# Performance work log

Measured on AMD Instinct MI355X. Metric: run time of the kernel, lower is better.

The kernel has to match this reference:

```python
import jax, jax.numpy as jnp
import numpy as np

B, SWIN_D, VIT_D, E, H = 16384, 768, 512, 1024, 4
HD = E // H  # 256


def setup_inputs() -> dict:
    key = jax.random.key(0)
    ks = jax.random.split(key, 12)
    s = lambda fan_in: 1.0 / np.sqrt(fan_in)
    return {
        "swin_feat": jax.random.normal(ks[0], (B, SWIN_D), jnp.float32),
        "vit_feat": jax.random.normal(ks[1], (B, VIT_D), jnp.float32),
        # outer projections (nn.Linear: y = x @ W.T + b)
        "Wq": jax.random.uniform(ks[2], (E, SWIN_D), jnp.float32, -s(SWIN_D), s(SWIN_D)),
        "bq": jax.random.uniform(ks[3], (E,), jnp.float32, -s(SWIN_D), s(SWIN_D)),
        "Wk": jax.random.uniform(ks[4], (E, VIT_D), jnp.float32, -s(VIT_D), s(VIT_D)),
        "bk": jax.random.uniform(ks[5], (E,), jnp.float32, -s(VIT_D), s(VIT_D)),
        "Wv": jax.random.uniform(ks[6], (E, VIT_D), jnp.float32, -s(VIT_D), s(VIT_D)),
        "bv": jax.random.uniform(ks[7], (E,), jnp.float32, -s(VIT_D), s(VIT_D)),
        # nn.MultiheadAttention internal in_proj (stacked q,k,v) and out_proj
        "in_proj_w": jax.random.uniform(ks[8], (3 * E, E), jnp.float32, -s(E), s(E)),
        "in_proj_b": jnp.zeros((3 * E,), jnp.float32),
        "Wo": jax.random.uniform(ks[9], (E, E), jnp.float32, -s(E), s(E)),
        "bo": jnp.zeros((E,), jnp.float32),
    }


def reference(swin_feat, vit_feat, Wq, bq, Wk, bk, Wv, bv, in_proj_w, in_proj_b, Wo, bo):
    # outer projections -> [B, E] (seq_len = 1, so the seq dim is implicit)
    q = swin_feat @ Wq.T + bq
    k = vit_feat @ Wk.T + bk
    v = vit_feat @ Wv.T + bv
    # MultiheadAttention in-projection (split stacked weight)
    Wiq, Wik, Wiv = in_proj_w[:E], in_proj_w[E:2 * E], in_proj_w[2 * E:]
    biq, bik, biv = in_proj_b[:E], in_proj_b[E:2 * E], in_proj_b[2 * E:]
    q2 = (q @ Wiq.T + biq).reshape(B, H, HD)
    k2 = (k @ Wik.T + bik).reshape(B, H, HD)
    v2 = (v @ Wiv.T + biv).reshape(B, H, HD)
    # attention with q_len = kv_len = 1
    scale = 1.0 / np.sqrt(HD)
    scores = jnp.einsum('bhd,bhd->bh', q2, k2) * scale        # [B, H]
    w = jax.nn.softmax(scores[..., None], axis=-1)             # softmax over 1 key -> ones
    attn = w * v2                                              # [B, H, HD]
    out = attn.reshape(B, E) @ Wo.T + bo                       # out-projection
    return out
```

## Files before the change

kernel.cpp:

```cpp
#include <hip/hip_runtime.h>
#include <stdint.h>
#include <stddef.h>

#define E_DIM 1024

typedef __bf16 v8bf __attribute__((ext_vector_type(8)));
typedef float v4f __attribute__((ext_vector_type(4)));

__device__ __forceinline__ unsigned short f2bf(float x) {
  unsigned int u = __builtin_bit_cast(unsigned int, x);
  u += 0x7fffu + ((u >> 16) & 1u);
  return (unsigned short)(u >> 16);
}

template <int RB>
__device__ __forceinline__ int swz(int r, int c) {
  if constexpr (RB >= 128) return c ^ ((r & 7) << 4);
  else return c;
}

template <int N>
__device__ __forceinline__ void waitcnt_vm() {
  static_assert(N == 0 || N == 4 || N == 8 || N == 12, "add literal");
  if constexpr (N == 0)  asm volatile("s_waitcnt vmcnt(0)" ::: "memory");
  if constexpr (N == 4)  asm volatile("s_waitcnt vmcnt(4)" ::: "memory");
  if constexpr (N == 8)  asm volatile("s_waitcnt vmcnt(8)" ::: "memory");
  if constexpr (N == 12) asm volatile("s_waitcnt vmcnt(12)" ::: "memory");
}

template <int ROWS, int BK>
__device__ __forceinline__ void stageg(const unsigned short* __restrict__ G, int g0,
                                       int ldg, int k0, char* L, int wid, int lane) {
  constexpr int RB = BK * 2;
  constexpr int ITERS = (ROWS * RB) / 4096;
#pragma unroll
  for (int it = 0; it < ITERS; ++it) {
    int lbase = it * 4096 + wid * 1024;
    int lin = lbase + lane * 16;
    int r = lin / RB, cb = lin % RB;
    int gcb = swz<RB>(r, cb);
    const char* g = (const char*)G + ((size_t)(g0 + r) * ldg + k0) * 2 + gcb;
    __builtin_amdgcn_global_load_lds((const __attribute__((address_space(1))) void*)g,
                                     (__attribute__((address_space(3))) void*)(L + lbase),
                                     16, 0, 0);
  }
}

template <int RB>
__device__ __forceinline__ v8bf frag_bf16(const char* L, int r, int kelem) {
  int o = swz<RB>(r, kelem * 2);
  return *(const v8bf*)(L + r * RB + o);
}

template <int BM, int BN, int BK, int FM, int FN>
__device__ __forceinline__ void compute_tile(const char* Al, const char* Bl,
                                             v4f (&acc)[FM][FN],
                                             int wr, int wc, int lr, int kg) {
  constexpr int RBA = BK * 2, RBB = BK * 2;
  constexpr int TMW = BM / 2, TNW = BN / 2;
#pragma unroll
  for (int kk = 0; kk < BK / 32; ++kk) {
    const int ke = kk * 32 + kg * 8;
    v8bf a[FM], b[FN];
#pragma unroll
    for (int mi = 0; mi < FM; ++mi)
      a[mi] = frag_bf16<RBA>(Al, wr * TMW + mi * 16 + lr, ke);
#pragma unroll
    for (int ni = 0; ni < FN; ++ni)
      b[ni] = frag_bf16<RBB>(Bl, wc * TNW + ni * 16 + lr, ke);
#pragma unroll
    for (int mi = 0; mi < FM; ++mi)
#pragma unroll
      for (int ni = 0; ni < FN; ++ni)
        acc[mi][ni] = __builtin_amdgcn_mfma_f32_16x16x32_bf16(a[mi], b[ni], acc[mi][ni], 0, 0, 0);
  }
}

__device__ __forceinline__ void cvt4(const float4* __restrict__ src,
                                     ushort4* __restrict__ dst, int i0) {
#pragma unroll
  for (int j = 0; j < 4; ++j) {
    int i = i0 + j * 256;
    float4 f = src[i];
    ushort4 u;
    u.x = f2bf(f.x); u.y = f2bf(f.y); u.z = f2bf(f.z); u.w = f2bf(f.w);
    dst[i] = u;
  }
}

__device__ __forceinline__ void mv4(const float* __restrict__ W, const float* __restrict__ x,
                                    const float* __restrict__ b, float* __restrict__ y,
                                    int blkrel, int tid) {
  int r = blkrel * 4 + (tid >> 6);
  int lane = tid & 63;
  float s = 0.f;
  for (int c = lane; c < 1024; c += 64) s += W[(size_t)r * 1024 + c] * x[c];
#pragma unroll
  for (int off = 32; off; off >>= 1) s += __shfl_down(s, off);
  if (lane == 0) y[r] = s + b[r];
}

__global__ __launch_bounds__(256) void prep1(const float* __restrict__ Wv,
                                             unsigned short* __restrict__ WvT,
                                             const float* __restrict__ Wiv,
                                             const float* __restrict__ bv,
                                             const float* __restrict__ biv,
                                             float* __restrict__ b1,
                                             unsigned short* __restrict__ Wivb) {
  int bid = blockIdx.x;
  int tid = threadIdx.x;
  if (bid < 512) {
    __shared__ float tile[32][33];
    const int R = 1024, C = 512;
    int nbx = C >> 5;
    int bx = bid % nbx, by = bid / nbx;
    int tx = tid & 31, ty = tid >> 5;
#pragma unroll
    for (int i = 0; i < 32; i += 8)
      tile[ty + i][tx] = Wv[(size_t)(by * 32 + ty + i) * C + bx * 32 + tx];
    __syncthreads();
#pragma unroll
    for (int i = 0; i < 32; i += 8)
      WvT[(size_t)(bx * 32 + ty + i) * R + by * 32 + tx] = f2bf(tile[tx][ty + i]);
  } else if (bid < 768) {
    mv4(Wiv, bv, biv, b1, bid - 512, tid);
  } else {
    cvt4((const float4*)Wiv, (ushort4*)Wivb, (bid - 768) * 1024 + tid);
  }
}

template <int BM, int BN, int BK, int FM, int FN, int OUTBF, int XCDSWZ>
__global__ __launch_bounds__(256) void gemm_cv(const unsigned short* __restrict__ A,
                                               const unsigned short* __restrict__ B,
                                               const float* __restrict__ bias,
                                               float* __restrict__ Cf,
                                               unsigned short* __restrict__ Cb,
                                               int M, int N, int K,
                                               const float* __restrict__ mvW,
                                               const float* __restrict__ mvx,
                                               const float* __restrict__ mvb,
                                               float* __restrict__ mvy, int nmv,
                                               const float* __restrict__ csrc1,
                                               unsigned short* __restrict__ cdst1,
                                               int cbase1, int ncv1,
                                               const float* __restrict__ csrc2,
                                               unsigned short* __restrict__ cdst2,
                                               int cbase2) {
  static_assert((BM + BN) * BK * 2 / 1024 / 4 == 4, "vmcnt literals assume 4 loads/tile/wave");
  __shared__ __align__(16) char Al0[BM * BK * 2];
  __shared__ __align__(16) char Al1[BM * BK * 2];
  __shared__ __align__(16) char Al2[BM * BK * 2];
  __shared__ __align__(16) char Al3[BM * BK * 2];
  __shared__ __align__(16) char Bl0[BN * BK * 2];
  __shared__ __align__(16) char Bl1[BN * BK * 2];
  __shared__ __align__(16) char Bl2[BN * BK * 2];
  __shared__ __align__(16) char Bl3[BN * BK * 2];
  const int nbn = N / BN;
  const int ngemm = nbn * (M / BM);
  int bid = blockIdx.x;
  const int tid = threadIdx.x;

  if (bid >= ngemm) {
    int rel = bid - ngemm;
    if (rel < nmv) {
      mv4(mvW, mvx, mvb, mvy, rel, tid);
    } else if (rel < nmv + ncv1) {
      cvt4((const float4*)csrc1, (ushort4*)cdst1, (cbase1 + rel - nmv) * 1024 + tid);
    } else {
      cvt4((const float4*)csrc2, (ushort4*)cdst2, (cbase2 + rel - nmv - ncv1) * 1024 + tid);
    }
    return;
  }

  int bm_i, bn_i;
  if (XCDSWZ) {
    int x = bid & 7, j = bid >> 3;
    bm_i = x + ((j >> 3) << 3);
    bn_i = j & 7;
  } else {
    bm_i = bid / nbn;
    bn_i = bid % nbn;
  }
  const int bm0 = bm_i * BM, bn0 = bn_i * BN;

  constexpr int TMW = BM / 2, TNW = BN / 2;
  const int lane = tid & 63;
  const int wid = tid >> 6;
  const int wr = wid >> 1, wc = wid & 1;
  const int lr = lane & 15;
  const int kg = lane >> 4;

  v4f acc[FM][FN];
#pragma unroll
  for (int i = 0; i < FM; ++i)
#pragma unroll
    for (int j = 0; j < FN; ++j) acc[i][j] = 0.f;

  const int NT = K / BK;

  stageg<BM, BK>(A, bm0, K, 0 * BK, Al0, wid, lane);
  stageg<BN, BK>(B, bn0, K, 0 * BK, Bl0, wid, lane);
  stageg<BM, BK>(A, bm0, K, 1 * BK, Al1, wid, lane);
  stageg<BN, BK>(B, bn0, K, 1 * BK, Bl1, wid, lane);
  stageg<BM, BK>(A, bm0, K, 2 * BK, Al2, wid, lane);
  stageg<BN, BK>(B, bn0, K, 2 * BK, Bl2, wid, lane);

#define GEMM_PHASE(CA, CB, SA, SB, TNXT, W)                              \
  waitcnt_vm<W>();                                                       \
  __builtin_amdgcn_s_barrier();                                          \
  __builtin_amdgcn_sched_barrier(0);                                     \
  if ((TNXT) < NT) {                                                     \
    stageg<BM, BK>(A, bm0, K, (TNXT)*BK, SA, wid, lane);                 \
    stageg<BN, BK>(B, bn0, K, (TNXT)*BK, SB, wid, lane);                 \
  }                                                                      \
  __builtin_amdgcn_s_setprio(1);                                         \
  compute_tile<BM, BN, BK, FM, FN>(CA, CB, acc, wr, wc, lr, kg);         \
  __builtin_amdgcn_s_setprio(0);                                         \
  __builtin_amdgcn_sched_barrier(0);

  for (int t = 0; t + 8 <= NT; t += 4) {
    GEMM_PHASE(Al0, Bl0, Al3, Bl3, t + 3, 8)
    GEMM_PHASE(Al1, Bl1, Al0, Bl0, t + 4, 8)
    GEMM_PHASE(Al2, Bl2, Al1, Bl1, t + 5, 8)
    GEMM_PHASE(Al3, Bl3, Al2, Bl2, t + 6, 8)
  }
  GEMM_PHASE(Al0, Bl0, Al3, Bl3, NT - 1, 8)
  GEMM_PHASE(Al1, Bl1, Al0, Bl0, NT, 8)
  GEMM_PHASE(Al2, Bl2, Al1, Bl1, NT, 4)
  GEMM_PHASE(Al3, Bl3, Al2, Bl2, NT, 0)
#undef GEMM_PHASE

#pragma unroll
  for (int ni = 0; ni < FN; ++ni) {
    int col = bn0 + wc * TNW + ni * 16 + lr;
    float bz = bias ? bias[col] : 0.f;
#pragma unroll
    for (int mi = 0; mi < FM; ++mi) {
      int row0 = bm0 + wr * TMW + mi * 16 + kg * 4;
#pragma unroll
      for (int r = 0; r < 4; ++r) {
        float v = acc[mi][ni][r] + bz;
        if (OUTBF) Cb[(size_t)(row0 + r) * N + col] = f2bf(v);
        else       Cf[(size_t)(row0 + r) * N + col] = v;
      }
    }
  }
}

extern "C" void kernel_launch(void* const* d_in, const int* in_sizes, int n_in,
                              void* d_out, int out_size, void* d_ws, size_t ws_size,
                              hipStream_t stream) {
  const float* vit = (const float*)d_in[1];
  const float* Wv  = (const float*)d_in[6];
  const float* bv  = (const float*)d_in[7];
  const float* ipw = (const float*)d_in[8];
  const float* ipb = (const float*)d_in[9];
  const float* Wo  = (const float*)d_in[10];
  const float* bo  = (const float*)d_in[11];
  const float* Wiv = ipw + 2 * E_DIM * E_DIM;
  const float* biv = ipb + 2 * E_DIM;

  char* ws = (char*)d_ws;
  unsigned short* Xb   = (unsigned short*)(ws);
  unsigned short* Wivb = (unsigned short*)(ws + (16 << 20));
  unsigned short* Wob  = (unsigned short*)(ws + (18 << 20));
  unsigned short* WvTb = (unsigned short*)(ws + (20 << 20));
  unsigned short* Ttb  = (unsigned short*)(ws + (21 << 20));
  unsigned short* Wcb  = (unsigned short*)(ws + (22 << 20));
  float* b1 = (float*)(ws + (23 << 20));
  float* bc = (float*)(ws + (23 << 20) + 4096);

  prep1<<<1024, 256, 0, stream>>>(Wv, WvTb, Wiv, bv, biv, b1, Wivb);

  gemm_cv<64, 64, 64, 2, 2, 1, 0><<<128 + 256 + 256 + 1024, 256, 0, stream>>>(
      WvTb, Wivb, nullptr, nullptr, Ttb, 512, 1024, 1024,
      Wo, b1, bo, bc, 256,
      Wo, Wob, 0, 256,
      vit, Xb, 0);

  gemm_cv<64, 64, 64, 2, 2, 1, 0><<<128 + 1024, 256, 0, stream>>>(
      Wob, Ttb, nullptr, nullptr, Wcb, 1024, 512, 1024,
      nullptr, nullptr, nullptr, nullptr, 0,
      vit, Xb, 1024, 1024,
      vit, Xb, 0);

  gemm_cv<128, 128, 32, 4, 4, 0, 1><<<1024, 256, 0, stream>>>(
      Xb, Wcb, bc, (float*)d_out, nullptr, 16384, 1024, 512,
      nullptr, nullptr, nullptr, nullptr, 0,
      nullptr, nullptr, 0, 0,
      nullptr, nullptr, 0);
}
```

Measured before the change: 59.00 us.

## Reduce GEMM LDS pipeline from four to three stages with fully unrolled fixed-K schedule

Drops the fourth LDS buffer for A and B, so the prefetch depth goes from three tiles ahead to two. The K loop is fully unrolled for exactly 16 tiles, with compile-time staging guards. The smaller shared-memory footprint may let more blocks fit per CU, at the cost of less latency hiding per block. It also hardcodes K/BK == 16, which breaks any call with a different K.

```diff
diff --git a/kernel.cpp b/kernel.cpp
--- a/kernel.cpp
+++ b/kernel.cpp
@@ -21,11 +21,10 @@
 
 template <int N>
 __device__ __forceinline__ void waitcnt_vm() {
-  static_assert(N == 0 || N == 4 || N == 8 || N == 12, "add literal");
-  if constexpr (N == 0)  asm volatile("s_waitcnt vmcnt(0)" ::: "memory");
-  if constexpr (N == 4)  asm volatile("s_waitcnt vmcnt(4)" ::: "memory");
-  if constexpr (N == 8)  asm volatile("s_waitcnt vmcnt(8)" ::: "memory");
-  if constexpr (N == 12) asm volatile("s_waitcnt vmcnt(12)" ::: "memory");
+  static_assert(N == 0 || N == 4 || N == 8, "add literal");
+  if constexpr (N == 0) asm volatile("s_waitcnt vmcnt(0)" ::: "memory");
+  if constexpr (N == 4) asm volatile("s_waitcnt vmcnt(4)" ::: "memory");
+  if constexpr (N == 8) asm volatile("s_waitcnt vmcnt(8)" ::: "memory");
 }
 
 template <int ROWS, int BK>
@@ -150,11 +149,9 @@
   __shared__ __align__(16) char Al0[BM * BK * 2];
   __shared__ __align__(16) char Al1[BM * BK * 2];
   __shared__ __align__(16) char Al2[BM * BK * 2];
-  __shared__ __align__(16) char Al3[BM * BK * 2];
   __shared__ __align__(16) char Bl0[BN * BK * 2];
   __shared__ __align__(16) char Bl1[BN * BK * 2];
   __shared__ __align__(16) char Bl2[BN * BK * 2];
-  __shared__ __align__(16) char Bl3[BN * BK * 2];
   const int nbn = N / BN;
   const int ngemm = nbn * (M / BM);
   int bid = blockIdx.x;
@@ -196,39 +193,42 @@
 #pragma unroll
     for (int j = 0; j < FN; ++j) acc[i][j] = 0.f;
 
-  const int NT = K / BK;
 
   stageg<BM, BK>(A, bm0, K, 0 * BK, Al0, wid, lane);
   stageg<BN, BK>(B, bn0, K, 0 * BK, Bl0, wid, lane);
   stageg<BM, BK>(A, bm0, K, 1 * BK, Al1, wid, lane);
   stageg<BN, BK>(B, bn0, K, 1 * BK, Bl1, wid, lane);
-  stageg<BM, BK>(A, bm0, K, 2 * BK, Al2, wid, lane);
-  stageg<BN, BK>(B, bn0, K, 2 * BK, Bl2, wid, lane);
-
-#define GEMM_PHASE(CA, CB, SA, SB, TNXT, W)                              \
+
+#define GP(CA, CB, SA, SB, TN, W)                                        \
   waitcnt_vm<W>();                                                       \
   __builtin_amdgcn_s_barrier();                                          \
   __builtin_amdgcn_sched_barrier(0);                                     \
-  if ((TNXT) < NT) {                                                     \
-    stageg<BM, BK>(A, bm0, K, (TNXT)*BK, SA, wid, lane);                 \
-    stageg<BN, BK>(B, bn0, K, (TNXT)*BK, SB, wid, lane);                 \
+  if constexpr ((TN) < 16) {                                             \
+    stageg<BM, BK>(A, bm0, K, (TN)*BK, SA, wid, lane);                   \
+    stageg<BN, BK>(B, bn0, K, (TN)*BK, SB, wid, lane);                   \
   }                                                                      \
   __builtin_amdgcn_s_setprio(1);                                         \
   compute_tile<BM, BN, BK, FM, FN>(CA, CB, acc, wr, wc, lr, kg);         \
   __builtin_amdgcn_s_setprio(0);                                         \
   __builtin_amdgcn_sched_barrier(0);
 
-  for (int t = 0; t + 8 <= NT; t += 4) {
-    GEMM_PHASE(Al0, Bl0, Al3, Bl3, t + 3, 8)
-    GEMM_PHASE(Al1, Bl1, Al0, Bl0, t + 4, 8)
-    GEMM_PHASE(Al2, Bl2, Al1, Bl1, t + 5, 8)
-    GEMM_PHASE(Al3, Bl3, Al2, Bl2, t + 6, 8)
-  }
-  GEMM_PHASE(Al0, Bl0, Al3, Bl3, NT - 1, 8)
-  GEMM_PHASE(Al1, Bl1, Al0, Bl0, NT, 8)
-  GEMM_PHASE(Al2, Bl2, Al1, Bl1, NT, 4)
-  GEMM_PHASE(Al3, Bl3, Al2, Bl2, NT, 0)
-#undef GEMM_PHASE
+  GP(Al0, Bl0, Al2, Bl2, 2, 4)
+  GP(Al1, Bl1, Al0, Bl0, 3, 4)
+  GP(Al2, Bl2, Al1, Bl1, 4, 4)
+  GP(Al0, Bl0, Al2, Bl2, 5, 4)
+  GP(Al1, Bl1, Al0, Bl0, 6, 4)
+  GP(Al2, Bl2, Al1, Bl1, 7, 4)
+  GP(Al0, Bl0, Al2, Bl2, 8, 4)
+  GP(Al1, Bl1, Al0, Bl0, 9, 4)
+  GP(Al2, Bl2, Al1, Bl1, 10, 4)
+  GP(Al0, Bl0, Al2, Bl2, 11, 4)
+  GP(Al1, Bl1, Al0, Bl0, 12, 4)
+  GP(Al2, Bl2, Al1, Bl1, 13, 4)
+  GP(Al0, Bl0, Al2, Bl2, 14, 4)
+  GP(Al1, Bl1, Al0, Bl0, 15, 4)
+  GP(Al2, Bl2, Al1, Bl1, 16, 4)
+  GP(Al0, Bl0, Al2, Bl2, 16, 0)
+#undef GP
 
 #pragma unroll
   for (int ni = 0; ni < FN; ++ni) {
```

New measurement: 60.51 us. +2.6%, slower.

## Add dedicated double-buffered 128x128x64 GEMM kernel for final projection

Applied to the files above, without the earlier changes.

The final 16384x1024x512 GEMM moves from the generic templated kernel to a specialised kernel. It uses 64-wide K tiles, two LDS buffers per operand, and fully unrolled stages with explicit vmcnt waits, barriers and setprio around the compute. The block index is remapped so that groups of 8 M-tiles share N-tiles, for better L2 reuse. The goal is to hide global load latency and cut loop overhead, at the cost of 64KB of LDS per block, which can lower occupancy.

```diff
diff --git a/kernel.cpp b/kernel.cpp
--- a/kernel.cpp
+++ b/kernel.cpp
@@ -247,6 +247,74 @@
   }
 }
 
+__global__ __launch_bounds__(256) void gemm_k4(const unsigned short* __restrict__ A,
+                                               const unsigned short* __restrict__ B,
+                                               const float* __restrict__ bias,
+                                               float* __restrict__ C,
+                                               int M, int N, int K) {
+  __shared__ __align__(16) char Al0[128 * 128];
+  __shared__ __align__(16) char Al1[128 * 128];
+  __shared__ __align__(16) char Bl0[128 * 128];
+  __shared__ __align__(16) char Bl1[128 * 128];
+  const int tid = threadIdx.x;
+  const int lane = tid & 63, wid = tid >> 6;
+  const int wr = wid >> 1, wc = wid & 1;
+  const int lr = lane & 15, kg = lane >> 4;
+
+  int bid = blockIdx.x;
+  int x = bid & 7, j = bid >> 3;
+  const int bm0 = (x + ((j >> 3) << 3)) * 128;
+  const int bn0 = (j & 7) * 128;
+
+  v4f acc[4][4];
+#pragma unroll
+  for (int i = 0; i < 4; ++i)
+#pragma unroll
+    for (int jj = 0; jj < 4; ++jj) acc[i][jj] = 0.f;
+
+  stageg<128, 64>(A, bm0, K, 0, Al0, wid, lane);
+  stageg<128, 64>(B, bn0, K, 0, Bl0, wid, lane);
+  stageg<128, 64>(A, bm0, K, 64, Al1, wid, lane);
+  stageg<128, 64>(B, bn0, K, 64, Bl1, wid, lane);
+
+#define K4P(CA, CB, TN2, W)                                              \
+  waitcnt_vm<W>();                                                       \
+  __builtin_amdgcn_s_barrier();                                          \
+  __builtin_amdgcn_sched_barrier(0);                                     \
+  __builtin_amdgcn_s_setprio(1);                                         \
+  compute_tile<128, 128, 64, 4, 4>(CA, CB, acc, wr, wc, lr, kg);         \
+  __builtin_amdgcn_s_setprio(0);                                         \
+  __builtin_amdgcn_sched_barrier(0);                                     \
+  __builtin_amdgcn_s_barrier();                                          \
+  if constexpr ((TN2) < 8) {                                             \
+    stageg<128, 64>(A, bm0, K, (TN2)*64, CA, wid, lane);                 \
+    stageg<128, 64>(B, bn0, K, (TN2)*64, CB, wid, lane);                 \
+  }
+
+  K4P(Al0, Bl0, 2, 8)
+  K4P(Al1, Bl1, 3, 8)
+  K4P(Al0, Bl0, 4, 8)
+  K4P(Al1, Bl1, 5, 8)
+  K4P(Al0, Bl0, 6, 8)
+  K4P(Al1, Bl1, 7, 8)
+  K4P(Al0, Bl0, 8, 8)
+  K4P(Al1, Bl1, 8, 0)
+#undef K4P
+
+#pragma unroll
+  for (int ni = 0; ni < 4; ++ni) {
+    int col = bn0 + wc * 64 + ni * 16 + lr;
+    float bz = bias[col];
+#pragma unroll
+    for (int mi = 0; mi < 4; ++mi) {
+      int row0 = bm0 + wr * 64 + mi * 16 + kg * 4;
+#pragma unroll
+      for (int r = 0; r < 4; ++r)
+        C[(size_t)(row0 + r) * N + col] = acc[mi][ni][r] + bz;
+    }
+  }
+}
+
 extern "C" void kernel_launch(void* const* d_in, const int* in_sizes, int n_in,
                               void* d_out, int out_size, void* d_ws, size_t ws_size,
                               hipStream_t stream) {
@@ -284,9 +352,5 @@
       vit, Xb, 1024, 1024,
       vit, Xb, 0);
 
-  gemm_cv<128, 128, 32, 4, 4, 0, 1><<<1024, 256, 0, stream>>>(
-      Xb, Wcb, bc, (float*)d_out, nullptr, 16384, 1024, 512,
-      nullptr, nullptr, nullptr, nullptr, 0,
-      nullptr, nullptr, 0, 0,
-      nullptr, nullptr, 0);
-}
+  gemm_k4<<<1024, 256, 0, stream>>>(Xb, Wcb, bc, (float*)d_out, 16384, 1024, 512);
+}
```

Result: faster. 56.29 us, median of 2 (-4.6%).
